# Optimization experiments

Hardware: AMD Instinct MI355X
Metric: run time of the kernel (lower is better)

## Reference

```python
import jax, jax.numpy as jnp
import numpy as np

B, T, D = 2, 2048, 768
H, DH = 12, 64  # heads, head_dim; H*DH == D


def setup_inputs() -> dict:
    key = jax.random.key(0)
    ks = jax.random.split(key, 9)
    s = 0.02  # small init scale like GPT-2
    return {
        "x": jax.random.normal(ks[0], (B, T, D), dtype=jnp.float32),
        "Wq": jax.random.normal(ks[1], (D, H * DH), dtype=jnp.float32) * s,
        "bq": jax.random.normal(ks[2], (H * DH,), dtype=jnp.float32) * s,
        "Wk": jax.random.normal(ks[3], (D, H * DH), dtype=jnp.float32) * s,
        "bk": jax.random.normal(ks[4], (H * DH,), dtype=jnp.float32) * s,
        "Wv": jax.random.normal(ks[5], (D, H * DH), dtype=jnp.float32) * s,
        "bv": jax.random.normal(ks[6], (H * DH,), dtype=jnp.float32) * s,
        "Wo": jax.random.normal(ks[7], (H * DH, H * DH), dtype=jnp.float32) * s,
        "bo": jax.random.normal(ks[8], (H * DH,), dtype=jnp.float32) * s,
    }


def reference(x, Wq, bq, Wk, bk, Wv, bv, Wo, bo):
    b, t, _ = x.shape
    # projections -> [b, t, H, DH] -> [b, H, t, DH]
    q = (x @ Wq + bq).reshape(b, t, H, DH).transpose(0, 2, 1, 3)
    k = (x @ Wk + bk).reshape(b, t, H, DH).transpose(0, 2, 1, 3)
    v = (x @ Wv + bv).reshape(b, t, H, DH).transpose(0, 2, 1, 3)
    # full O(T^2) score matrix, matching the naive torch module
    scores = jnp.einsum("bhqd,bhkd->bhqk", q, k)
    causal = jnp.tril(jnp.ones((t, t), dtype=bool))  # True = keep
    scores = jnp.where(causal, scores, -jnp.inf)
    weights = jax.nn.softmax(scores / jnp.sqrt(jnp.float32(DH)), axis=-1)
    # dropout with p=0.0 is identity
    ctx = jnp.einsum("bhqk,bhkd->bhqd", weights, v)
    ctx = ctx.transpose(0, 2, 1, 3).reshape(b, t, H * DH)
    return ctx @ Wo + bo
```

## Files before the change

kernel.cpp:

```cpp
#include <hip/hip_runtime.h>
#include <hip/hip_bf16.h>
#include <math.h>

typedef unsigned short u16;
typedef unsigned int u32;
typedef __attribute__((ext_vector_type(8))) short short8v;
typedef __attribute__((ext_vector_type(4))) float f32x4;
typedef __attribute__((ext_vector_type(16))) float f32x16;

#define BB 2
#define TT 2048
#define DD 768
#define HH 12
#define DHH 64
#define MM 4096
#define NSLOT 36
#define QSC 0.18033688f

#define SWZ(r, kb) (((r) * 128) + ((kb) ^ (((r) & 7) << 4)))

typedef __attribute__((address_space(1))) void gas_void;
typedef __attribute__((address_space(3))) void las_void;
#define GLL(g, l) __builtin_amdgcn_global_load_lds((gas_void*)(g), (las_void*)(l), 16, 0, 0)

__device__ const unsigned char SLOT_QT[36] = {
    7,7,7,7,7,7,7, 6,6,6,6,6,6, 5,5,5,5,5, 4,4,4,4, 3,3,3, 2,2, 1,
    7,6,5,4,3,2,1,0};
__device__ const unsigned char SLOT_C[36] = {
    0,1,2,3,4,5,6, 0,1,2,3,4,5, 0,1,2,3,4, 0,1,2,3, 0,1,2, 0,1, 0,
    7,6,5,4,3,2,1,0};
__device__ const unsigned char BASEF[8] = {0, 27, 25, 22, 18, 13, 7, 0};

__device__ __forceinline__ u16 f2bf(float f) {
    union { float f; unsigned u; } v; v.f = f;
    unsigned r = v.u + 0x7fff + ((v.u >> 16) & 1);
    return (u16)(r >> 16);
}
__device__ __forceinline__ u32 pkpair(float a, float b) {
    union { __hip_bfloat162 h; u32 u; } v;
    v.h = __float22bfloat162_rn(make_float2(a, b));
    return v.u;
}
__device__ __forceinline__ float fexp2(float x) {
#if __has_builtin(__builtin_amdgcn_exp2f)
    return __builtin_amdgcn_exp2f(x);
#else
    return exp2f(x);
#endif
}
__device__ __forceinline__ float bfhi(u32 p) {
    union { u32 u; float f; } v; v.u = p & 0xffff0000u; return v.f;
}
__device__ __forceinline__ float bflo(u32 p) {
    union { u32 u; float f; } v; v.u = p << 16; return v.f;
}

__global__ __launch_bounds__(256) void convert_x(const float* __restrict__ x,
                                                 u16* __restrict__ xb) {
    const int i = blockIdx.x * 256 + threadIdx.x;
    const float4 v = ((const float4*)x)[i];
    union { u16 s[4]; uint2 u; } o;
    o.s[0] = f2bf(v.x); o.s[1] = f2bf(v.y); o.s[2] = f2bf(v.z); o.s[3] = f2bf(v.w);
    ((uint2*)xb)[i] = o.u;
}

__global__ __launch_bounds__(256) void transpose_cvt(
    const float* __restrict__ W0, const float* __restrict__ W1,
    const float* __restrict__ W2, const float* __restrict__ W3,
    u16* __restrict__ T0, u16* __restrict__ T1,
    u16* __restrict__ T2, u16* __restrict__ T3)
{
    const int z = blockIdx.z;
    const float* __restrict__ W = (z == 0) ? W0 : (z == 1) ? W1 : (z == 2) ? W2 : W3;
    u16* __restrict__ T = (z == 0) ? T0 : (z == 1) ? T1 : (z == 2) ? T2 : T3;

    __shared__ float tile[64][65];
    const int k0 = blockIdx.x * 64, n0 = blockIdx.y * 64;
    const int t = threadIdx.x;
    const int rr = t >> 4, c4 = (t & 15) * 4;

    #pragma unroll
    for (int j = 0; j < 4; ++j) {
        const int r = rr + j * 16;
        const float4 v = *(const float4*)&W[(size_t)(k0 + r) * DD + n0 + c4];
        tile[r][c4 + 0] = v.x; tile[r][c4 + 1] = v.y;
        tile[r][c4 + 2] = v.z; tile[r][c4 + 3] = v.w;
    }
    __syncthreads();
    #pragma unroll
    for (int j = 0; j < 4; ++j) {
        const int r = rr + j * 16;
        union { u16 s[4]; uint2 u; } o;
        #pragma unroll
        for (int jj = 0; jj < 4; ++jj) o.s[jj] = f2bf(tile[c4 + jj][r]);
        *(uint2*)&T[(size_t)(n0 + r) * DD + k0 + c4] = o.u;
    }
}

__global__ __launch_bounds__(256) void gemm_bt(
    const u16* __restrict__ A,
    const u16* __restrict__ Bt0, const u16* __restrict__ Bt1, const u16* __restrict__ Bt2,
    const float* __restrict__ b0, const float* __restrict__ b1, const float* __restrict__ b2,
    u16* __restrict__ oQ, u16* __restrict__ oK, u16* __restrict__ oVt,
    float* __restrict__ oF, int mode_base)
{
    const int mode = mode_base + blockIdx.z;
    const u16* __restrict__ Bt = (mode == 1) ? Bt1 : (mode == 2) ? Bt2 : Bt0;
    const float* __restrict__ bias = (mode == 1) ? b1 : (mode == 2) ? b2 : b0;

    __shared__ __attribute__((aligned(16))) u16 As[128 * 64];
    __shared__ __attribute__((aligned(16))) u16 Bs[128 * 64];

    const int tid = threadIdx.x, lane = tid & 63, w = tid >> 6;
    const int wr = w >> 1, wc = w & 1;
    const int lr = lane >> 4, lc = lane & 15;
    const int m0 = blockIdx.x * 128, n0 = blockIdx.y * 128;
    const int srcoff = 16 * ((lane & 7) ^ (lane >> 3));

    f32x4 acc[4][4];
    #pragma unroll
    for (int m = 0; m < 4; ++m)
        #pragma unroll
        for (int n = 0; n < 4; ++n) acc[m][n] = (f32x4){0.f, 0.f, 0.f, 0.f};

    #pragma unroll 1
    for (int k0 = 0; k0 < DD; k0 += 64) {
        __syncthreads();
        #pragma unroll
        for (int i = 0; i < 4; ++i) {
            const int r = w * 32 + i * 8 + (lane >> 3);
            GLL((const char*)A  + ((size_t)(m0 + r) * DD + k0) * 2 + srcoff,
                (char*)As + w * 4096 + i * 1024);
            GLL((const char*)Bt + ((size_t)(n0 + r) * DD + k0) * 2 + srcoff,
                (char*)Bs + w * 4096 + i * 1024);
        }
        __syncthreads();
        #pragma unroll
        for (int s = 0; s < 2; ++s) {
            short8v af[4], bf[4];
            #pragma unroll
            for (int m = 0; m < 4; ++m)
                af[m] = *(const short8v*)((const char*)As +
                         SWZ(wr * 64 + m * 16 + lc, s * 64 + lr * 16));
            #pragma unroll
            for (int n = 0; n < 4; ++n)
                bf[n] = *(const short8v*)((const char*)Bs +
                         SWZ(wc * 64 + n * 16 + lc, s * 64 + lr * 16));
            #pragma unroll
            for (int m = 0; m < 4; ++m)
                #pragma unroll
                for (int n = 0; n < 4; ++n)
                    acc[m][n] = __builtin_amdgcn_mfma_f32_16x16x32_bf16(
                        af[m], bf[n], acc[m][n], 0, 0, 0);
        }
    }

    #pragma unroll
    for (int n = 0; n < 4; ++n) {
        const int ng = n0 + wc * 64 + n * 16 + lc;
        const float bv = bias[ng];
        #pragma unroll
        for (int m = 0; m < 4; ++m) {
            const int mg0 = m0 + wr * 64 + m * 16 + lr * 4;
            if (mode == 3) {
                #pragma unroll
                for (int r = 0; r < 4; ++r)
                    oF[(size_t)(mg0 + r) * DD + ng] = acc[m][n][r] + bv;
            } else if (mode == 2) {
                const int bb = mg0 >> 11, tp = mg0 & 2047;
                const int h = ng >> 6, d = ng & 63;
                const size_t idx = (size_t)(bb * HH + h) * (TT * DHH)
                                 + (tp >> 6) * 4096 + ((tp >> 3) & 7) * 512
                                 + d * 8 + (tp & 7);
                union { u16 s[4]; uint2 u; } o;
                #pragma unroll
                for (int r = 0; r < 4; ++r) o.s[r] = f2bf(acc[m][n][r] + bv);
                *(uint2*)&oVt[idx] = o.u;
            } else if (mode == 1) {
                const int h = ng >> 6, d = ng & 63;
                #pragma unroll
                for (int r = 0; r < 4; ++r) {
                    const int mg = mg0 + r;
                    const int bb = mg >> 11, tp = mg & 2047;
                    oK[(size_t)(bb * HH + h) * (TT * DHH)
                       + (tp >> 6) * 4096 + (d >> 3) * 512 + (tp & 63) * 8 + (d & 7)] =
                        f2bf(acc[m][n][r] + bv);
                }
            } else {
                const int h = ng >> 6, d = ng & 63;
                #pragma unroll
                for (int r = 0; r < 4; ++r) {
                    const int mg = mg0 + r;
                    const int bb = mg >> 11, tp = mg & 2047;
                    oQ[((size_t)(bb * HH + h) * TT + tp) * DHH + d] =
                        f2bf((acc[m][n][r] + bv) * QSC);
                }
            }
        }
    }
}

__global__ __launch_bounds__(512) void attn_fwd(
    const u16* __restrict__ qb, const u16* __restrict__ kbf,
    const u16* __restrict__ vtb, u16* __restrict__ partO,
    float* __restrict__ partL)
{
    __shared__ __attribute__((aligned(16))) unsigned char smem[32768];

    const int bid = blockIdx.x;
    const int sp = bid / 24;
    const int bh = bid - sp * 24;
    const int qt = SLOT_QT[sp], c = SLOT_C[sp];
    const int kts = c * 4;
    const int kte = kts + 4;

    const int tid = threadIdx.x, lane = tid & 63, w = tid >> 6;
    const int l31 = lane & 31, hi = lane >> 5;

    short8v aq[4];
    {
        const u16* qrow = qb + ((size_t)bh * TT + qt * 256 + w * 32 + l31) * DHH;
        #pragma unroll
        for (int s4 = 0; s4 < 4; ++s4)
            aq[s4] = *(const short8v*)(qrow + s4 * 16 + hi * 8);
    }

    const char* kbase = (const char*)kbf + (size_t)bh * (TT * DHH * 2);
    const char* vbase = (const char*)vtb + (size_t)bh * (TT * DHH * 2);

#define STAGE(kt2, bufi) do {                                                  \
        const char* kb_ = kbase + (size_t)(kt2) * 8192;                        \
        const char* vb_ = vbase + (size_t)(kt2) * 8192;                        \
        const int off_ = w * 1024;                                             \
        GLL(kb_ + off_ + lane * 16,                                            \
            (char*)smem + (bufi) * 8192 + off_);                               \
        GLL(vb_ + off_ + lane * 16,                                            \
            (char*)smem + 16384 + (bufi) * 8192 + off_);                       \
    } while (0)

    f32x16 accO[2];
    #pragma unroll
    for (int i = 0; i < 16; ++i) { accO[0][i] = 0.f; accO[1][i] = 0.f; }
    float lreg = 0.f;

    STAGE(kts, 0);
    __syncthreads();

    int cur = 0;
    const int qmin = qt * 256 + w * 32;
    #pragma unroll 1
    for (int kt = kts; kt < kte; ++kt) {
        if (kt + 1 < kte) STAGE(kt + 1, cur ^ 1);

        if (kt * 64 <= qmin + 31) {
            const unsigned char* Kb = smem + cur * 8192;
            const unsigned char* Vb = smem + 16384 + cur * 8192;

            f32x16 st[2];
            #pragma unroll
            for (int i = 0; i < 16; ++i) { st[0][i] = 0.f; st[1][i] = 0.f; }
            __builtin_amdgcn_s_setprio(1);
            #pragma unroll
            for (int s4 = 0; s4 < 4; ++s4) {
                #pragma unroll
                for (int kf = 0; kf < 2; ++kf) {
                    const short8v ak = *(const short8v*)(Kb +
                        (s4 * 2 + hi) * 1024 + (kf * 32 + l31) * 16);
                    st[kf] = __builtin_amdgcn_mfma_f32_32x32x16_bf16(ak, aq[s4], st[kf], 0, 0, 0);
                }
            }
            __builtin_amdgcn_s_setprio(0);

            if (kt * 64 + 63 > qmin) {
                const int rowrel = qmin + l31 - kt * 64;
                #pragma unroll
                for (int kf = 0; kf < 2; ++kf)
                    #pragma unroll
                    for (int reg = 0; reg < 16; ++reg) {
                        const int kloc = kf * 32 + (reg & 3) + 8 * (reg >> 2) + 4 * hi;
                        if (kloc > rowrel) st[kf][reg] = -3.0e38f;
                    }
            }

            float rs4[4] = {0.f, 0.f, 0.f, 0.f};
            #pragma unroll
            for (int kf = 0; kf < 2; ++kf)
                #pragma unroll
                for (int reg = 0; reg < 16; ++reg) {
                    const float p = fexp2(st[kf][reg]);
                    st[kf][reg] = p;
                    rs4[reg & 3] += p;
                }
            float rs = (rs4[0] + rs4[1]) + (rs4[2] + rs4[3]);
            {
                u32 a, b;
                union { float f; u32 u; } cv; cv.f = rs;
                a = cv.u; b = cv.u;
                asm volatile("v_permlane32_swap_b32 %0, %1" : "+v"(a), "+v"(b));
                union { u32 u; float f; } pa, pb; pa.u = a; pb.u = b;
                const float partner = hi ? pa.f : pb.f;
                rs += partner;
            }
            lreg += rs;

            __builtin_amdgcn_s_setprio(1);
            #pragma unroll
            for (int ka = 0; ka < 4; ++ka) {
                const int kf = ka >> 1;
                const int rb0 = 4 * ((ka & 1) * 2);
                const int rb1 = 4 * ((ka & 1) * 2 + 1);
                u32 P0 = pkpair(st[kf][rb0 + 0], st[kf][rb0 + 1]);
                u32 P1 = pkpair(st[kf][rb0 + 2], st[kf][rb0 + 3]);
                u32 Q0 = pkpair(st[kf][rb1 + 0], st[kf][rb1 + 1]);
                u32 Q1 = pkpair(st[kf][rb1 + 2], st[kf][rb1 + 3]);
                asm volatile("v_permlane32_swap_b32 %0, %1" : "+v"(P0), "+v"(Q0));
                asm volatile("v_permlane32_swap_b32 %0, %1" : "+v"(P1), "+v"(Q1));
                union { u32 wd[4]; short8v v; } u;
                u.wd[0] = P0; u.wd[1] = P1; u.wd[2] = Q0; u.wd[3] = Q1;
                #pragma unroll
                for (int dc = 0; dc < 2; ++dc) {
                    const short8v bv = *(const short8v*)(Vb +
                        (ka * 2 + hi) * 1024 + (dc * 32 + l31) * 16);
                    accO[dc] = __builtin_amdgcn_mfma_f32_32x32x16_bf16(u.v, bv, accO[dc], 0, 0, 0);
                }
            }
            __builtin_amdgcn_s_setprio(0);
        }

        __syncthreads();
        cur ^= 1;
    }

    const int gslot = bh * NSLOT + sp;
    if (hi == 0)
        partL[(size_t)gslot * 256 + w * 32 + l31] = lreg;
    u16* po = partO + (size_t)gslot * 16384;
    #pragma unroll
    for (int reg = 0; reg < 16; ++reg) {
        const int qrow = (reg & 3) + 8 * (reg >> 2) + 4 * hi;
        #pragma unroll
        for (int dc = 0; dc < 2; ++dc)
            po[(w * 32 + qrow) * 64 + dc * 32 + l31] = f2bf(accO[dc][reg]);
    }
#undef STAGE
}

__global__ __launch_bounds__(512) void attn_combine(
    const u16* __restrict__ partO, const float* __restrict__ partL,
    u16* __restrict__ ctx)
{
    const int bid = blockIdx.x;
    const int qt = bid / 24, bh = bid - qt * 24;
    const int b = bh / HH, h = bh - b * HH;
    const int tid = threadIdx.x, q = tid >> 1, half = tid & 1;

    float lsum = 0.f;
    float acc[32];
    #pragma unroll
    for (int j = 0; j < 32; ++j) acc[j] = 0.f;

#define ACCUM(gs) do {                                                         \
        lsum += partL[(size_t)(gs) * 256 + q];                                 \
        const u16* po_ = partO + (size_t)(gs) * 16384 + q * 64 + half * 32;    \
        _Pragma("unroll")                                                      \
        for (int v_ = 0; v_ < 4; ++v_) {                                       \
            const uint4 pk = *(const uint4*)(po_ + v_ * 8);                    \
            acc[v_*8+0] += bflo(pk.x); acc[v_*8+1] += bfhi(pk.x);              \
            acc[v_*8+2] += bflo(pk.y); acc[v_*8+3] += bfhi(pk.y);              \
            acc[v_*8+4] += bflo(pk.z); acc[v_*8+5] += bfhi(pk.z);              \
            acc[v_*8+6] += bflo(pk.w); acc[v_*8+7] += bfhi(pk.w);              \
        }                                                                      \
    } while (0)

    const int basef = bh * NSLOT + BASEF[qt];
    #pragma unroll 1
    for (int cc = 0; cc < qt; ++cc) ACCUM(basef + cc);
    ACCUM(bh * NSLOT + (35 - qt));
#undef ACCUM

    const float inv = 1.f / lsum;
    u16* dst = ctx + (size_t)(b * TT + qt * 256 + q) * DD + h * 64 + half * 32;
    #pragma unroll
    for (int v = 0; v < 4; ++v) {
        uint4 o;
        o.x = pkpair(acc[v*8+0] * inv, acc[v*8+1] * inv);
        o.y = pkpair(acc[v*8+2] * inv, acc[v*8+3] * inv);
        o.z = pkpair(acc[v*8+4] * inv, acc[v*8+5] * inv);
        o.w = pkpair(acc[v*8+6] * inv, acc[v*8+7] * inv);
        *(uint4*)(dst + v * 8) = o;
    }
}

extern "C" void kernel_launch(void* const* d_in, const int* in_sizes, int n_in,
                              void* d_out, int out_size, void* d_ws, size_t ws_size,
                              hipStream_t stream) {
    (void)in_sizes; (void)n_in; (void)out_size; (void)ws_size;
    const float* x  = (const float*)d_in[0];
    const float* Wq = (const float*)d_in[1];
    const float* bq = (const float*)d_in[2];
    const float* Wk = (const float*)d_in[3];
    const float* bk = (const float*)d_in[4];
    const float* Wv = (const float*)d_in[5];
    const float* bv = (const float*)d_in[6];
    const float* Wo = (const float*)d_in[7];
    const float* bo = (const float*)d_in[8];
    float* out = (float*)d_out;

    u16* xb    = (u16*)d_ws;
    u16* WtQ   = xb + (size_t)MM * DD;
    u16* WtK   = WtQ + (size_t)DD * DD;
    u16* WtV   = WtK + (size_t)DD * DD;
    u16* WtO   = WtV + (size_t)DD * DD;
    u16* qbuf  = WtO + (size_t)DD * DD;
    u16* kbuf  = qbuf + (size_t)MM * DD;
    u16* vtbuf = kbuf + (size_t)MM * DD;
    u16* ctxb  = vtbuf + (size_t)MM * DD;
    u16* pO    = ctxb + (size_t)MM * DD;
    float* pL  = (float*)(pO + (size_t)24 * NSLOT * 16384);

    convert_x<<<3072, 256, 0, stream>>>(x, xb);
    transpose_cvt<<<dim3(12, 12, 4), 256, 0, stream>>>(Wq, Wk, Wv, Wo, WtQ, WtK, WtV, WtO);
    gemm_bt<<<dim3(32, 6, 3), 256, 0, stream>>>(xb, WtQ, WtK, WtV, bq, bk, bv,
                                                qbuf, kbuf, vtbuf, nullptr, 0);
    attn_fwd<<<dim3(24 * NSLOT), 512, 0, stream>>>(qbuf, kbuf, vtbuf, pO, pL);
    attn_combine<<<dim3(192), 512, 0, stream>>>(pO, pL, ctxb);
    gemm_bt<<<dim3(32, 6, 1), 256, 0, stream>>>(ctxb, WtO, nullptr, nullptr, bo, nullptr, nullptr,
                                                nullptr, nullptr, nullptr, out, 3);
}
```

Before: 107.0 us.

## Double-buffer GEMM LDS tiles and merge prep conversion kernels into one launch

The GEMM now keeps two LDS buffers per operand and issues the async global-to-LDS loads for the next k-tile before computing on the current one, so there is one barrier per iteration instead of two. This is meant to hide global load latency behind the MFMA work. The x-conversion and weight transpose/convert kernels are also merged into a single launch with a flat grid, which removes one kernel launch. The cost is doubled LDS use (64KB per block), which can lower occupancy. Correctness relies on waitcnt handling of the async LDS loads before the barrier.

```diff
diff --git a/kernel.cpp b/kernel.cpp
--- a/kernel.cpp
+++ b/kernel.cpp
@@ -55,30 +55,34 @@
     union { u32 u; float f; } v; v.u = p << 16; return v.f;
 }
 
-__global__ __launch_bounds__(256) void convert_x(const float* __restrict__ x,
-                                                 u16* __restrict__ xb) {
-    const int i = blockIdx.x * 256 + threadIdx.x;
-    const float4 v = ((const float4*)x)[i];
-    union { u16 s[4]; uint2 u; } o;
-    o.s[0] = f2bf(v.x); o.s[1] = f2bf(v.y); o.s[2] = f2bf(v.z); o.s[3] = f2bf(v.w);
-    ((uint2*)xb)[i] = o.u;
-}
-
-__global__ __launch_bounds__(256) void transpose_cvt(
+__global__ __launch_bounds__(256) void prep(
+    const float* __restrict__ x, u16* __restrict__ xb,
     const float* __restrict__ W0, const float* __restrict__ W1,
     const float* __restrict__ W2, const float* __restrict__ W3,
     u16* __restrict__ T0, u16* __restrict__ T1,
     u16* __restrict__ T2, u16* __restrict__ T3)
 {
-    const int z = blockIdx.z;
+    __shared__ float tile[64][65];
+    const int bid = blockIdx.x;
+    const int t = threadIdx.x;
+
+    if (bid < 3072) {
+        const int i = bid * 256 + t;
+        const float4 v = ((const float4*)x)[i];
+        union { u16 s[4]; uint2 u; } o;
+        o.s[0] = f2bf(v.x); o.s[1] = f2bf(v.y); o.s[2] = f2bf(v.z); o.s[3] = f2bf(v.w);
+        ((uint2*)xb)[i] = o.u;
+        return;
+    }
+
+    const int idx = bid - 3072;
+    const int z = idx / 144;
+    const int r2 = idx - z * 144;
+    const int k0 = (r2 / 12) * 64, n0 = (r2 % 12) * 64;
     const float* __restrict__ W = (z == 0) ? W0 : (z == 1) ? W1 : (z == 2) ? W2 : W3;
     u16* __restrict__ T = (z == 0) ? T0 : (z == 1) ? T1 : (z == 2) ? T2 : T3;
 
-    __shared__ float tile[64][65];
-    const int k0 = blockIdx.x * 64, n0 = blockIdx.y * 64;
-    const int t = threadIdx.x;
     const int rr = t >> 4, c4 = (t & 15) * 4;
-
     #pragma unroll
     for (int j = 0; j < 4; ++j) {
         const int r = rr + j * 16;
@@ -108,8 +112,8 @@
     const u16* __restrict__ Bt = (mode == 1) ? Bt1 : (mode == 2) ? Bt2 : Bt0;
     const float* __restrict__ bias = (mode == 1) ? b1 : (mode == 2) ? b2 : b0;
 
-    __shared__ __attribute__((aligned(16))) u16 As[128 * 64];
-    __shared__ __attribute__((aligned(16))) u16 Bs[128 * 64];
+    __shared__ __attribute__((aligned(16))) unsigned char AsB[2][16384];
+    __shared__ __attribute__((aligned(16))) unsigned char BsB[2][16384];
 
     const int tid = threadIdx.x, lane = tid & 63, w = tid >> 6;
     const int wr = w >> 1, wc = w & 1;
@@ -117,34 +121,41 @@
     const int m0 = blockIdx.x * 128, n0 = blockIdx.y * 128;
     const int srcoff = 16 * ((lane & 7) ^ (lane >> 3));
 
+#define GSTAGE(k0_, bufi) do {                                                 \
+        _Pragma("unroll")                                                      \
+        for (int i_ = 0; i_ < 4; ++i_) {                                       \
+            const int r_ = w * 32 + i_ * 8 + (lane >> 3);                      \
+            GLL((const char*)A  + ((size_t)(m0 + r_) * DD + (k0_)) * 2 + srcoff,\
+                (char*)AsB[bufi] + w * 4096 + i_ * 1024);                      \
+            GLL((const char*)Bt + ((size_t)(n0 + r_) * DD + (k0_)) * 2 + srcoff,\
+                (char*)BsB[bufi] + w * 4096 + i_ * 1024);                      \
+        }                                                                      \
+    } while (0)
+
     f32x4 acc[4][4];
     #pragma unroll
     for (int m = 0; m < 4; ++m)
         #pragma unroll
         for (int n = 0; n < 4; ++n) acc[m][n] = (f32x4){0.f, 0.f, 0.f, 0.f};
 
+    GSTAGE(0, 0);
+    __syncthreads();
+
+    int cur = 0;
     #pragma unroll 1
     for (int k0 = 0; k0 < DD; k0 += 64) {
-        __syncthreads();
-        #pragma unroll
-        for (int i = 0; i < 4; ++i) {
-            const int r = w * 32 + i * 8 + (lane >> 3);
-            GLL((const char*)A  + ((size_t)(m0 + r) * DD + k0) * 2 + srcoff,
-                (char*)As + w * 4096 + i * 1024);
-            GLL((const char*)Bt + ((size_t)(n0 + r) * DD + k0) * 2 + srcoff,
-                (char*)Bs + w * 4096 + i * 1024);
-        }
-        __syncthreads();
+        if (k0 + 64 < DD) GSTAGE(k0 + 64, cur ^ 1);
+
         #pragma unroll
         for (int s = 0; s < 2; ++s) {
             short8v af[4], bf[4];
             #pragma unroll
             for (int m = 0; m < 4; ++m)
-                af[m] = *(const short8v*)((const char*)As +
+                af[m] = *(const short8v*)((const char*)AsB[cur] +
                          SWZ(wr * 64 + m * 16 + lc, s * 64 + lr * 16));
             #pragma unroll
             for (int n = 0; n < 4; ++n)
-                bf[n] = *(const short8v*)((const char*)Bs +
+                bf[n] = *(const short8v*)((const char*)BsB[cur] +
                          SWZ(wc * 64 + n * 16 + lc, s * 64 + lr * 16));
             #pragma unroll
             for (int m = 0; m < 4; ++m)
@@ -153,7 +164,11 @@
                     acc[m][n] = __builtin_amdgcn_mfma_f32_16x16x32_bf16(
                         af[m], bf[n], acc[m][n], 0, 0, 0);
         }
-    }
+
+        __syncthreads();
+        cur ^= 1;
+    }
+#undef GSTAGE
 
     #pragma unroll
     for (int n = 0; n < 4; ++n) {
@@ -418,8 +433,7 @@
     u16* pO    = ctxb + (size_t)MM * DD;
     float* pL  = (float*)(pO + (size_t)24 * NSLOT * 16384);
 
-    convert_x<<<3072, 256, 0, stream>>>(x, xb);
-    transpose_cvt<<<dim3(12, 12, 4), 256, 0, stream>>>(Wq, Wk, Wv, Wo, WtQ, WtK, WtV, WtO);
+    prep<<<dim3(3648), 256, 0, stream>>>(x, xb, Wq, Wk, Wv, Wo, WtQ, WtK, WtV, WtO);
     gemm_bt<<<dim3(32, 6, 3), 256, 0, stream>>>(xb, WtQ, WtK, WtV, bq, bk, bv,
                                                 qbuf, kbuf, vtbuf, nullptr, 0);
     attn_fwd<<<dim3(24 * NSLOT), 512, 0, stream>>>(qbuf, kbuf, vtbuf, pO, pL);
```

New measurement: 99.57 us. 6.9% less time.
